# Kernel optimization log

Hardware: AMD Instinct MI355X
Metric: run time of the kernel (lower is better)

Reference implementation:

```python
import jax, jax.numpy as jnp
import numpy as np

B, T, D, H = 4, 2048, 1024, 16
DH = D // H


def setup_inputs() -> dict:
    key = jax.random.key(0)
    ks = jax.random.split(key, 11)
    s = 1.0 / np.sqrt(D)
    return {
        "q": jax.random.normal(ks[0], (B, T, D), jnp.float32),
        "k": jax.random.normal(ks[1], (B, T, D), jnp.float32),
        "v": jax.random.normal(ks[2], (B, T, D), jnp.float32),
        "Wq": jax.random.normal(ks[3], (D, D), jnp.float32) * s,
        "bq": jax.random.normal(ks[4], (D,), jnp.float32) * s,
        "Wk": jax.random.normal(ks[5], (D, D), jnp.float32) * s,
        "bk": jax.random.normal(ks[6], (D,), jnp.float32) * s,
        "Wv": jax.random.normal(ks[7], (D, D), jnp.float32) * s,
        "bv": jax.random.normal(ks[8], (D,), jnp.float32) * s,
        "Wo": jax.random.normal(ks[9], (D, D), jnp.float32) * s,
        "bo": jax.random.normal(ks[10], (D,), jnp.float32) * s,
    }


def _heads(x):
    # (B, T, D) -> (B, H, T, DH)
    return x.reshape(B, T, H, DH).transpose(0, 2, 1, 3)


def reference(q, k, v, Wq, bq, Wk, bk, Wv, bv, Wo, bo):
    qh = _heads(q @ Wq + bq)
    kh = _heads(k @ Wk + bk)
    vh = _heads(v @ Wv + bv)
    scale = 1.0 / np.sqrt(DH).astype(np.float32)
    # full (B, H, T, T) score matrix, as in the original module
    scores = jnp.einsum("bhqd,bhkd->bhqk", qh, kh) * scale
    causal = jnp.tril(jnp.ones((T, T), dtype=bool))  # keep j <= i (causal intent)
    scores = jnp.where(causal, scores, -jnp.inf)
    attn = jax.nn.softmax(scores, axis=-1)
    ctx = jnp.einsum("bhqk,bhkd->bhqd", attn, vh)
    ctx = ctx.transpose(0, 2, 1, 3).reshape(B, T, D)
    return ctx @ Wo + bo
```

## Files before the change

### kernel.cpp

```cpp
#include <hip/hip_runtime.h>
#include <hip/hip_bf16.h>

#define NB 4
#define NT 2048
#define ND 1024
#define NH 16
#define NDH 64
#define NM (NB*NT)

typedef __bf16 bf16_t;
typedef bf16_t bf16x4 __attribute__((ext_vector_type(4)));
typedef bf16_t bf16x8 __attribute__((ext_vector_type(8)));
typedef float f32x2 __attribute__((ext_vector_type(2)));
typedef float f32x4 __attribute__((ext_vector_type(4)));
typedef unsigned int u32x4 __attribute__((ext_vector_type(4)));

__device__ __forceinline__ void gload_lds16(const bf16_t* g, bf16_t* l) {
  __builtin_amdgcn_global_load_lds(
      (const __attribute__((address_space(1))) unsigned int*)g,
      (__attribute__((address_space(3))) unsigned int*)l, 16, 0, 0);
}

__device__ __forceinline__ f32x2 lo2(f32x4 v) { return __builtin_shufflevector(v, v, 0, 1); }
__device__ __forceinline__ f32x2 hi2(f32x4 v) { return __builtin_shufflevector(v, v, 2, 3); }

__device__ __forceinline__ float exp2_hw(float x) {
  float r;
  asm("v_exp_f32 %0, %1" : "=v"(r) : "v"(x));
  return r;
}

__global__ void transpose_cvt4(const float* __restrict__ w0, const float* __restrict__ w1,
                               const float* __restrict__ w2, const float* __restrict__ w3,
                               bf16_t* __restrict__ o0, bf16_t* __restrict__ o1,
                               bf16_t* __restrict__ o2, bf16_t* __restrict__ o3) {
  __shared__ float tile[32][33];
  const float* in = blockIdx.z == 0 ? w0 : blockIdx.z == 1 ? w1 : blockIdx.z == 2 ? w2 : w3;
  bf16_t* out     = blockIdx.z == 0 ? o0 : blockIdx.z == 1 ? o1 : blockIdx.z == 2 ? o2 : o3;
  int n0 = blockIdx.x * 32, k0 = blockIdx.y * 32;
  int tx = threadIdx.x & 31, ty = threadIdx.x >> 5;
  #pragma unroll
  for (int r = ty; r < 32; r += 8)
    tile[r][tx] = in[(size_t)(k0 + r) * ND + n0 + tx];
  __syncthreads();
  #pragma unroll
  for (int r = ty; r < 32; r += 8)
    out[(size_t)(n0 + r) * ND + k0 + tx] = (bf16_t)tile[tx][r];
}

__global__ void cvt3(const float* __restrict__ q, const float* __restrict__ k,
                     const float* __restrict__ v, bf16_t* __restrict__ oq,
                     bf16_t* __restrict__ ok, bf16_t* __restrict__ ov) {
  const float* in = blockIdx.y == 0 ? q : blockIdx.y == 1 ? k : v;
  bf16_t* out     = blockIdx.y == 0 ? oq : blockIdx.y == 1 ? ok : ov;
  int i = blockIdx.x * 256 + threadIdx.x;
  float4 vv = ((const float4*)in)[i];
  bf16x4 o;
  o[0] = (bf16_t)vv.x; o[1] = (bf16_t)vv.y; o[2] = (bf16_t)vv.z; o[3] = (bf16_t)vv.w;
  ((bf16x4*)out)[i] = o;
}


#define GEMM8_CORE(Aptr, Btptr)                                                     \
  const int K = ND;                                                                 \
  const int tid = threadIdx.x, lane = tid & 63, wid = tid >> 6;                     \
  const int wm = wid >> 2, wn = wid & 3;                                            \
  const int lrow = lane & 15, lg = lane >> 4, rb = lg << 2;                         \
  const int tm = blockIdx.y * 128, tn = blockIdx.x * 256;                           \
  const int d0 = tid * 16, d1 = 8192 + tid * 16;                                    \
  const int r0s = d0 >> 7, r1s = d1 >> 7;                                           \
  const int cb0 = (d0 & 127) ^ ((r0s & 7) << 4);                                    \
  const int cb1 = (d1 & 127) ^ ((r1s & 7) << 4);                                    \
  const int e0 = d0 >> 1, e1 = d1 >> 1;                                             \
  const bf16_t* aC0 = (Aptr) + (size_t)(tm + r0s) * K + (cb0 >> 1);                 \
  const bf16_t* aC1 = (Aptr) + (size_t)(tm + r1s) * K + (cb1 >> 1);                 \
  const bf16_t* b0C0 = (Btptr) + (size_t)(tn + r0s) * K + (cb0 >> 1);               \
  const bf16_t* b0C1 = (Btptr) + (size_t)(tn + r1s) * K + (cb1 >> 1);               \
  const bf16_t* b1C0 = b0C0 + (size_t)128 * K;                                      \
  const bf16_t* b1C1 = b0C1 + (size_t)128 * K;                                      \
  const int swzk = (lrow & 7) << 4;                                                 \
  const int kc0 = (lg * 16) ^ swzk;                                                 \
  const int kc1 = (64 + lg * 16) ^ swzk;                                            \
  const int aBase = wm * 8192 + lrow * 128;                                         \
  const int bBase = (wn & 1) * 8192 + lrow * 128;                                   \
  f32x4 acc[4][4];                                                                  \
  _Pragma("unroll")                                                                 \
  for (int m = 0; m < 4; ++m)                                                       \
    _Pragma("unroll")                                                               \
    for (int n = 0; n < 4; ++n) {                                                   \
      f32x4 zz = {0.f, 0.f, 0.f, 0.f};                                              \
      acc[m][n] = zz;                                                               \
    }                                                                               \
                           \
  gload_lds16(aC0,  &S[0][0][0] + e0); gload_lds16(aC1,  &S[0][0][0] + e1);         \
  gload_lds16(b0C0, &S[0][1][0] + e0); gload_lds16(b0C1, &S[0][1][0] + e1);         \
  gload_lds16(b1C0, &S[0][2][0] + e0); gload_lds16(b1C1, &S[0][2][0] + e1);         \
  gload_lds16(b0C0 + 64, &S[1][1][0] + e0); gload_lds16(b0C1 + 64, &S[1][1][0] + e1);\
  gload_lds16(b1C0 + 64, &S[1][2][0] + e0); gload_lds16(b1C1 + 64, &S[1][2][0] + e1);\
  asm volatile("s_waitcnt vmcnt(4)\n\ts_barrier" ::: "memory");                     \
  const int NS = K / 64;                                                            \
  _Pragma("unroll 1")                                                               \
  for (int s = 0; s < NS; ++s) {                                                    \
    const int b = s & 1;                                                            \
    const char* aReg = (const char*)&S[b][0][0];                                    \
    const char* bReg = (const char*)&S[b][1 + (wn >> 1)][0];                        \
                \
    bf16x8 bfr[4][2];                                                               \
    _Pragma("unroll")                                                               \
    for (int n = 0; n < 4; ++n) {                                                   \
      bfr[n][0] = *(const bf16x8*)(bReg + n * 2048 + bBase + kc0);                  \
      bfr[n][1] = *(const bf16x8*)(bReg + n * 2048 + bBase + kc1);                  \
    }                                                                               \
    bf16x8 afrA[2][2];                                                              \
    afrA[0][0] = *(const bf16x8*)(aReg + 0 * 2048 + aBase + kc0);                   \
    afrA[0][1] = *(const bf16x8*)(aReg + 0 * 2048 + aBase + kc1);                   \
    afrA[1][0] = *(const bf16x8*)(aReg + 1 * 2048 + aBase + kc0);                   \
    afrA[1][1] = *(const bf16x8*)(aReg + 1 * 2048 + aBase + kc1);                   \
    if (s + 1 < NS) {                                                               \
      gload_lds16(aC0 + (s + 1) * 64, &S[b ^ 1][0][0] + e0);                        \
      gload_lds16(aC1 + (s + 1) * 64, &S[b ^ 1][0][0] + e1);                        \
    }                                                                               \
    asm volatile("s_barrier" ::: "memory");                                         \
    __builtin_amdgcn_s_setprio(1);                                                  \
    _Pragma("unroll")                                                               \
    for (int mm = 0; mm < 2; ++mm)                                                  \
      _Pragma("unroll")                                                             \
      for (int n = 0; n < 4; ++n)                                                   \
        _Pragma("unroll")                                                           \
        for (int kk = 0; kk < 2; ++kk)                                              \
          acc[mm][n] = __builtin_amdgcn_mfma_f32_16x16x32_bf16(                     \
              afrA[mm][kk], bfr[n][kk], acc[mm][n], 0, 0, 0);                       \
    __builtin_amdgcn_s_setprio(0);                                                  \
    asm volatile("s_waitcnt lgkmcnt(0)\n\ts_barrier" ::: "memory");                 \
                            \
    bf16x8 afrB[2][2];                                                              \
    afrB[0][0] = *(const bf16x8*)(aReg + 2 * 2048 + aBase + kc0);                   \
    afrB[0][1] = *(const bf16x8*)(aReg + 2 * 2048 + aBase + kc1);                   \
    afrB[1][0] = *(const bf16x8*)(aReg + 3 * 2048 + aBase + kc0);                   \
    afrB[1][1] = *(const bf16x8*)(aReg + 3 * 2048 + aBase + kc1);                   \
    if (s + 2 < NS) {                                                               \
      gload_lds16(b0C0 + (s + 2) * 64, &S[b][1][0] + e0);                           \
      gload_lds16(b0C1 + (s + 2) * 64, &S[b][1][0] + e1);                           \
      gload_lds16(b1C0 + (s + 2) * 64, &S[b][2][0] + e0);                           \
      gload_lds16(b1C1 + (s + 2) * 64, &S[b][2][0] + e1);                           \
    }                                                                               \
    asm volatile("s_barrier" ::: "memory");                                         \
    __builtin_amdgcn_s_setprio(1);                                                  \
    _Pragma("unroll")                                                               \
    for (int mm = 0; mm < 2; ++mm)                                                  \
      _Pragma("unroll")                                                             \
      for (int n = 0; n < 4; ++n)                                                   \
        _Pragma("unroll")                                                           \
        for (int kk = 0; kk < 2; ++kk)                                              \
          acc[2 + mm][n] = __builtin_amdgcn_mfma_f32_16x16x32_bf16(                 \
              afrB[mm][kk], bfr[n][kk], acc[2 + mm][n], 0, 0, 0);                   \
    __builtin_amdgcn_s_setprio(0);                                                  \
    if (s < NS - 2)                                                                 \
      asm volatile("s_waitcnt vmcnt(4) lgkmcnt(0)\n\ts_barrier" ::: "memory");      \
    else if (s == NS - 2)                                                           \
      asm volatile("s_waitcnt vmcnt(0) lgkmcnt(0)\n\ts_barrier" ::: "memory");      \
    else                                                                            \
      asm volatile("s_waitcnt lgkmcnt(0)" ::: "memory");                            \
  }

__global__ __launch_bounds__(512, 2) void gemm8_qkv(
    const bf16_t* __restrict__ Aq, const bf16_t* __restrict__ Ak, const bf16_t* __restrict__ Av,
    const bf16_t* __restrict__ Bq, const bf16_t* __restrict__ Bk, const bf16_t* __restrict__ Bv,
    const float* __restrict__ bq, const float* __restrict__ bk, const float* __restrict__ bv,
    bf16_t* __restrict__ Qh, bf16_t* __restrict__ Kh, bf16_t* __restrict__ Vt,
    float qscale) {
  __shared__ bf16_t S[2][3][8192];
  const int z = blockIdx.z;
  const bf16_t* A    = z == 0 ? Aq : z == 1 ? Ak : Av;
  const bf16_t* Bt   = z == 0 ? Bq : z == 1 ? Bk : Bv;
  const float*  bias = z == 0 ? bq : z == 1 ? bk : bv;
  const float   scale = z == 0 ? qscale : 1.0f;
  bf16_t* outp = z == 0 ? Qh : z == 1 ? Kh : Vt;

  GEMM8_CORE(A, Bt)

  #pragma unroll
  for (int n = 0; n < 4; ++n) {
    const int ncol = tn + wn * 64 + n * 16 + lrow;
    const float bv = bias[ncol];
    const int h = ncol >> 6, dh = ncol & (NDH - 1);
    #pragma unroll
    for (int m = 0; m < 4; ++m) {
      const int m0 = tm + wm * 64 + m * 16 + rb;
      const int bb = m0 >> 11, t0 = m0 & (NT - 1);
      if (z == 2) {
        bf16x4 o;
        #pragma unroll
        for (int r = 0; r < 4; ++r) o[r] = (bf16_t)(acc[m][n][r] + bv);
        size_t idx = ((size_t)(bb * NH + h) * NDH + dh) * NT + t0;
        *(bf16x4*)(outp + idx) = o;
      } else {
        #pragma unroll
        for (int r = 0; r < 4; ++r) {
          float val = (acc[m][n][r] + bv) * scale;
          size_t idx = ((size_t)(bb * NH + h) * NT + t0 + r) * NDH + dh;
          outp[idx] = (bf16_t)val;
        }
      }
    }
  }
}

__global__ __launch_bounds__(512, 2) void gemm8_out(
    const bf16_t* __restrict__ A, const bf16_t* __restrict__ Bt,
    const float* __restrict__ bias, float* __restrict__ outp) {
  __shared__ bf16_t S[2][3][8192];

  GEMM8_CORE(A, Bt)

  #pragma unroll
  for (int n = 0; n < 4; ++n) {
    const int ncol = tn + wn * 64 + n * 16 + lrow;
    const float bv = bias[ncol];
    #pragma unroll
    for (int m = 0; m < 4; ++m) {
      const int m0 = tm + wm * 64 + m * 16 + rb;
      #pragma unroll
      for (int r = 0; r < 4; ++r)
        outp[(size_t)(m0 + r) * ND + ncol] = acc[m][n][r] + bv;
    }
  }
}

__device__ __forceinline__ bf16x8 lds_swz_read(const bf16_t* base, int row, int colb) {
  return *(const bf16x8*)((const char*)base + row * 128 + (colb ^ ((row & 7) << 4)));
}

#define CVTPK(lo, hi) ({ unsigned r_; \
  asm("v_cvt_pk_bf16_f32 %0, %1, %2" : "=v"(r_) : "v"(lo), "v"(hi)); r_; })

__global__ __launch_bounds__(256) void attn_kernel(
    const bf16_t* __restrict__ Qh, const bf16_t* __restrict__ Kh,
    const bf16_t* __restrict__ Vt, bf16_t* __restrict__ ctx) {
  __shared__ bf16_t Ks[2][64 * 64];
  __shared__ bf16_t Vs[2][64 * 64];
  const int tid  = threadIdx.x;
  const int lane = tid & 63;
  const int wid  = tid >> 6;

  const int work    = (blockIdx.x & 7) * 128 + (blockIdx.x >> 3);
  const int bh      = work >> 4;
  const int pairIdx = work & 15;
  const int b = bh >> 4, h = bh & 15;

  const bf16_t* Qbh = Qh + (size_t)bh * NT * NDH;
  const bf16_t* Kbh = Kh + (size_t)bh * NT * NDH;
  const bf16_t* Vbh = Vt + (size_t)bh * NDH * NT;

  const int lrow = lane & 15;
  const int lg   = lane >> 4;

  const char *kS0, *kS1, *vS0, *vS1;
  {
    int o0 = wid * 1024 + lane * 16;
    int o1 = 4096 + wid * 1024 + lane * 16;
    int r0_ = o0 >> 7, r1_ = o1 >> 7;
    kS0 = (const char*)Kbh + (o0 ^ ((r0_ & 7) << 4));
    kS1 = (const char*)Kbh + (o1 ^ ((r1_ & 7) << 4));
    int c0 = (o0 & 127) ^ ((r0_ & 7) << 4);
    int c1 = (o1 & 127) ^ ((r1_ & 7) << 4);
    vS0 = (const char*)Vbh + (size_t)r0_ * (NT * 2) + c0;
    vS1 = (const char*)Vbh + (size_t)r1_ * (NT * 2) + c1;
  }
  const int ldsOff = wid * 512;

  auto stage = [&](int t, int buf) {
    bf16_t* kb = Ks[buf];
    bf16_t* vb = Vs[buf];
    size_t kOff = (size_t)t * 8192;
    size_t vOff = (size_t)t * 128;
    gload_lds16((const bf16_t*)(kS0 + kOff), kb + ldsOff);
    gload_lds16((const bf16_t*)(kS1 + kOff), kb + 2048 + ldsOff);
    gload_lds16((const bf16_t*)(vS0 + vOff), vb + ldsOff);
    gload_lds16((const bf16_t*)(vS1 + vOff), vb + 2048 + ldsOff);
  };

  #pragma unroll 1
  for (int half = 0; half < 2; ++half) {
    const int qidx = half ? (31 - pairIdx) : pairIdx;
    const int r0   = qidx * 64 + wid * 16;
    const int qg   = r0 + lrow;

    bf16x8 qf0 = *(const bf16x8*)&Qbh[(size_t)(r0 + lrow) * NDH + lg * 8];
    bf16x8 qf1 = *(const bf16x8*)&Qbh[(size_t)(r0 + lrow) * NDH + 32 + lg * 8];

    float lsum = 0.f;
    f32x4 acc[4];
    #pragma unroll
    for (int d = 0; d < 4; ++d) { f32x4 z = {0.f, 0.f, 0.f, 0.f}; acc[d] = z; }

    __syncthreads();
    stage(0, 0);
    int cur = 0;

    #pragma unroll 1
    for (int t = 0; t <= qidx; ++t) {
      asm volatile("s_waitcnt vmcnt(0)\n\ts_barrier" ::: "memory");
      if (t < qidx) stage(t + 1, cur ^ 1);

      const bf16_t* ksCur = Ks[cur];
      const bf16_t* vsCur = Vs[cur];

      f32x4 sg[4];
      #pragma unroll
      for (int g = 0; g < 4; ++g) { f32x4 z = {0.f, 0.f, 0.f, 0.f}; sg[g] = z; }
      __builtin_amdgcn_s_setprio(1);
      #pragma unroll
      for (int g = 0; g < 4; ++g) {
        bf16x8 kfa = lds_swz_read(ksCur, g * 16 + lrow, lg * 16);
        sg[g] = __builtin_amdgcn_mfma_f32_16x16x32_bf16(kfa, qf0, sg[g], 0, 0, 0);
        bf16x8 kfb = lds_swz_read(ksCur, g * 16 + lrow, 64 + lg * 16);
        sg[g] = __builtin_amdgcn_mfma_f32_16x16x32_bf16(kfb, qf1, sg[g], 0, 0, 0);
      }
      __builtin_amdgcn_s_setprio(0);

      if (t == qidx) {
        const int jb = t * 64;
        #pragma unroll
        for (int g = 0; g < 4; ++g)
          #pragma unroll
          for (int r = 0; r < 4; ++r)
            if (jb + g * 16 + lg * 4 + r > qg) sg[g][r] = -1e30f;
      }

      #pragma unroll
      for (int g = 0; g < 4; ++g)
        #pragma unroll
        for (int r = 0; r < 4; ++r) sg[g][r] = exp2_hw(sg[g][r]);
      f32x2 s2 = (lo2(sg[0]) + hi2(sg[0])) + (lo2(sg[1]) + hi2(sg[1]));
      s2 += (lo2(sg[2]) + hi2(sg[2])) + (lo2(sg[3]) + hi2(sg[3]));
      lsum += s2[0] + s2[1];

      unsigned W00 = CVTPK(sg[0][0], sg[0][1]), W01 = CVTPK(sg[0][2], sg[0][3]);
      unsigned W10 = CVTPK(sg[1][0], sg[1][1]), W11 = CVTPK(sg[1][2], sg[1][3]);
      unsigned W20 = CVTPK(sg[2][0], sg[2][1]), W21 = CVTPK(sg[2][2], sg[2][3]);
      unsigned W30 = CVTPK(sg[3][0], sg[3][1]), W31 = CVTPK(sg[3][2], sg[3][3]);
      unsigned w00, w01, w02, w03, w10, w11, w12, w13;
      { unsigned a = W00, bb = W10;
        asm("v_permlane32_swap_b32 %0, %1" : "+v"(a), "+v"(bb));
        asm("v_permlane16_swap_b32 %0, %1" : "+v"(a), "+v"(bb));
        w00 = a; w02 = bb; }
      { unsigned a = W01, bb = W11;
        asm("v_permlane32_swap_b32 %0, %1" : "+v"(a), "+v"(bb));
        asm("v_permlane16_swap_b32 %0, %1" : "+v"(a), "+v"(bb));
        w01 = a; w03 = bb; }
      { unsigned a = W20, bb = W30;
        asm("v_permlane32_swap_b32 %0, %1" : "+v"(a), "+v"(bb));
        asm("v_permlane16_swap_b32 %0, %1" : "+v"(a), "+v"(bb));
        w10 = a; w12 = bb; }
      { unsigned a = W21, bb = W31;
        asm("v_permlane32_swap_b32 %0, %1" : "+v"(a), "+v"(bb));
        asm("v_permlane16_swap_b32 %0, %1" : "+v"(a), "+v"(bb));
        w11 = a; w13 = bb; }
      u32x4 c0 = {w00, w01, w02, w03};
      u32x4 c1 = {w10, w11, w12, w13};
      bf16x8 pf0 = __builtin_bit_cast(bf16x8, c0);
      bf16x8 pf1 = __builtin_bit_cast(bf16x8, c1);

      __builtin_amdgcn_s_setprio(1);
      #pragma unroll
      for (int d = 0; d < 4; ++d) {
        bf16x8 vf0 = lds_swz_read(vsCur, d * 16 + lrow, lg * 16);
        acc[d] = __builtin_amdgcn_mfma_f32_16x16x32_bf16(vf0, pf0, acc[d], 0, 0, 0);
        bf16x8 vf1 = lds_swz_read(vsCur, d * 16 + lrow, 64 + lg * 16);
        acc[d] = __builtin_amdgcn_mfma_f32_16x16x32_bf16(vf1, pf1, acc[d], 0, 0, 0);
      }
      __builtin_amdgcn_s_setprio(0);

      cur ^= 1;
    }

    float ps = lsum;
    ps += __shfl_xor(ps, 16);
    ps += __shfl_xor(ps, 32);
    float inv = 1.f / ps;
    f32x4 inv4 = {inv, inv, inv, inv};
    size_t orow = ((size_t)b * NT + qg) * ND + h * NDH;
    #pragma unroll
    for (int d2 = 0; d2 < 4; ++d2) {
      f32x4 vv = acc[d2] * inv4;
      bf16x4 o;
      #pragma unroll
      for (int r = 0; r < 4; ++r) o[r] = (bf16_t)vv[r];
      *(bf16x4*)&ctx[orow + d2 * 16 + lg * 4] = o;
    }
  }
}

extern "C" void kernel_launch(void* const* d_in, const int* in_sizes, int n_in,
                              void* d_out, int out_size, void* d_ws, size_t ws_size,
                              hipStream_t stream) {
  const float* q  = (const float*)d_in[0];
  const float* k  = (const float*)d_in[1];
  const float* v  = (const float*)d_in[2];
  const float* Wq = (const float*)d_in[3];
  const float* bq = (const float*)d_in[4];
  const float* Wk = (const float*)d_in[5];
  const float* bk = (const float*)d_in[6];
  const float* Wv = (const float*)d_in[7];
  const float* bv = (const float*)d_in[8];
  const float* Wo = (const float*)d_in[9];
  const float* bo = (const float*)d_in[10];
  float* out = (float*)d_out;

  char* ws = (char*)d_ws;
  const size_t szMK = (size_t)NM * ND * sizeof(bf16_t);
  const size_t szW  = (size_t)ND * ND * sizeof(bf16_t);
  bf16_t* Xq  = (bf16_t*)d_out;
  bf16_t* Xk  = Xq + (size_t)NM * ND;
  bf16_t* Xv  = (bf16_t*)(ws);
  bf16_t* ctx = (bf16_t*)(ws);
  bf16_t* Qh  = (bf16_t*)(ws + szMK);
  bf16_t* Kh  = (bf16_t*)(ws + 2 * szMK);
  bf16_t* Vt  = (bf16_t*)(ws + 3 * szMK);
  bf16_t* Wqt = (bf16_t*)(ws + 4 * szMK);
  bf16_t* Wkt = (bf16_t*)(ws + 4 * szMK + szW);
  bf16_t* Wvt = (bf16_t*)(ws + 4 * szMK + 2 * szW);
  bf16_t* Wot = (bf16_t*)(ws + 4 * szMK + 3 * szW);

  dim3 tb(256);
  transpose_cvt4<<<dim3(ND / 32, ND / 32, 4), tb, 0, stream>>>(Wq, Wk, Wv, Wo,
                                                               Wqt, Wkt, Wvt, Wot);

  const float qscale = 0.125f * 1.44269504f;

  cvt3<<<dim3(NM * ND / 4 / 256, 3), tb, 0, stream>>>(q, k, v, Xq, Xk, Xv);

  gemm8_qkv<<<dim3(ND / 256, NM / 128, 3), dim3(512), 0, stream>>>(
      Xq, Xk, Xv, Wqt, Wkt, Wvt, bq, bk, bv, Qh, Kh, Vt, qscale);

  attn_kernel<<<dim3(NB * NH * 16), tb, 0, stream>>>(Qh, Kh, Vt, ctx);

  gemm8_out<<<dim3(ND / 256, NM / 128), dim3(512), 0, stream>>>(ctx, Wot, bo, out);
}
```

Before: 183.3 us.

## Fuse fp32-to-bf16 input conversion into QKV projection GEMM A-tile loads

The separate cvt3 kernel, which wrote bf16 copies of q/k/v, is removed. The QKV GEMM now loads fp32 A tiles into registers, converts them with packed bf16 conversions, and stores them swizzled into LDS, with a two-stage register prefetch. This removes one full write and read of the bf16 activations plus a kernel launch. In exchange the GEMM reads twice as many A bytes from global memory, and register pressure in the inner loop goes up.

```diff
diff --git a/kernel.cpp b/kernel.cpp
--- a/kernel.cpp
+++ b/kernel.cpp
@@ -29,6 +29,9 @@
   asm("v_exp_f32 %0, %1" : "=v"(r) : "v"(x));
   return r;
 }
+
+#define CVTPK(lo, hi) ({ unsigned r_; \
+  asm("v_cvt_pk_bf16_f32 %0, %1, %2" : "=v"(r_) : "v"(lo), "v"(hi)); r_; })
 
 __global__ void transpose_cvt4(const float* __restrict__ w0, const float* __restrict__ w1,
                                const float* __restrict__ w2, const float* __restrict__ w3,
@@ -48,18 +51,171 @@
     out[(size_t)(n0 + r) * ND + k0 + tx] = (bf16_t)tile[tx][r];
 }
 
-__global__ void cvt3(const float* __restrict__ q, const float* __restrict__ k,
-                     const float* __restrict__ v, bf16_t* __restrict__ oq,
-                     bf16_t* __restrict__ ok, bf16_t* __restrict__ ov) {
-  const float* in = blockIdx.y == 0 ? q : blockIdx.y == 1 ? k : v;
-  bf16_t* out     = blockIdx.y == 0 ? oq : blockIdx.y == 1 ? ok : ov;
-  int i = blockIdx.x * 256 + threadIdx.x;
-  float4 vv = ((const float4*)in)[i];
-  bf16x4 o;
-  o[0] = (bf16_t)vv.x; o[1] = (bf16_t)vv.y; o[2] = (bf16_t)vv.z; o[3] = (bf16_t)vv.w;
-  ((bf16x4*)out)[i] = o;
-}
-
+__global__ __launch_bounds__(512, 2) void gemm8_qkv(
+    const float* __restrict__ Aq, const float* __restrict__ Ak, const float* __restrict__ Av,
+    const bf16_t* __restrict__ Bq, const bf16_t* __restrict__ Bk, const bf16_t* __restrict__ Bv,
+    const float* __restrict__ bq, const float* __restrict__ bk, const float* __restrict__ bv,
+    bf16_t* __restrict__ Qh, bf16_t* __restrict__ Kh, bf16_t* __restrict__ Vt,
+    float qscale) {
+  __shared__ bf16_t S[2][3][8192];
+  const int z = blockIdx.z;
+  const float*  A    = z == 0 ? Aq : z == 1 ? Ak : Av;
+  const bf16_t* Bt   = z == 0 ? Bq : z == 1 ? Bk : Bv;
+  const float*  bias = z == 0 ? bq : z == 1 ? bk : bv;
+  const float   scale = z == 0 ? qscale : 1.0f;
+  bf16_t* outp = z == 0 ? Qh : z == 1 ? Kh : Vt;
+
+  const int K = ND;
+  const int tid = threadIdx.x, lane = tid & 63, wid = tid >> 6;
+  const int wm = wid >> 2, wn = wid & 3;
+  const int lrow = lane & 15, lg = lane >> 4, rb = lg << 2;
+  const int tm = blockIdx.y * 128, tn = blockIdx.x * 256;
+
+  const int d0 = tid * 16, d1 = 8192 + tid * 16;
+  const int r0s = d0 >> 7, r1s = d1 >> 7;
+  const int cb0 = (d0 & 127) ^ ((r0s & 7) << 4);
+  const int cb1 = (d1 & 127) ^ ((r1s & 7) << 4);
+  const int e0 = d0 >> 1, e1 = d1 >> 1;
+  const bf16_t* b0C0 = Bt + (size_t)(tn + r0s) * K + (cb0 >> 1);
+  const bf16_t* b0C1 = Bt + (size_t)(tn + r1s) * K + (cb1 >> 1);
+  const bf16_t* b1C0 = b0C0 + (size_t)128 * K;
+  const bf16_t* b1C1 = b0C1 + (size_t)128 * K;
+
+  const int arow = tid >> 2;
+  const int acolf = (tid & 3) << 4;
+  const float* aF = A + (size_t)(tm + arow) * K + acolf;
+  const int aswz = (arow & 7) << 4;
+  const int wb0 = arow * 128 + ((((tid & 3) << 5))      ^ aswz);
+  const int wb1 = arow * 128 + ((((tid & 3) << 5) + 16) ^ aswz);
+
+  const int swzk = (lrow & 7) << 4;
+  const int kc0 = (lg * 16) ^ swzk;
+  const int kc1 = (64 + lg * 16) ^ swzk;
+  const int aBase = wm * 8192 + lrow * 128;
+  const int bBase = (wn & 1) * 8192 + lrow * 128;
+
+  f32x4 acc[4][4];
+  #pragma unroll
+  for (int m = 0; m < 4; ++m)
+    #pragma unroll
+    for (int n = 0; n < 4; ++n) {
+      f32x4 zz = {0.f, 0.f, 0.f, 0.f};
+      acc[m][n] = zz;
+    }
+
+  float4 ar0, ar1, ar2, ar3;
+  #define LOAD_ARX(off) do { const float4* ap_ = (const float4*)(aF + (off)); \
+    ar0 = ap_[0]; ar1 = ap_[1]; ar2 = ap_[2]; ar3 = ap_[3]; } while (0)
+  #define CVT_WRITE_A(dstBase) do { \
+    u32x4 c0_ = { CVTPK(ar0.x, ar0.y), CVTPK(ar0.z, ar0.w), \
+                  CVTPK(ar1.x, ar1.y), CVTPK(ar1.z, ar1.w) }; \
+    u32x4 c1_ = { CVTPK(ar2.x, ar2.y), CVTPK(ar2.z, ar2.w), \
+                  CVTPK(ar3.x, ar3.y), CVTPK(ar3.z, ar3.w) }; \
+    *(u32x4*)((char*)(dstBase) + wb0) = c0_; \
+    *(u32x4*)((char*)(dstBase) + wb1) = c1_; \
+  } while (0)
+
+  LOAD_ARX(0);
+  gload_lds16(b0C0, &S[0][1][0] + e0); gload_lds16(b0C1, &S[0][1][0] + e1);
+  gload_lds16(b1C0, &S[0][2][0] + e0); gload_lds16(b1C1, &S[0][2][0] + e1);
+  gload_lds16(b0C0 + 64, &S[1][1][0] + e0); gload_lds16(b0C1 + 64, &S[1][1][0] + e1);
+  gload_lds16(b1C0 + 64, &S[1][2][0] + e0); gload_lds16(b1C1 + 64, &S[1][2][0] + e1);
+  CVT_WRITE_A(&S[0][0][0]);
+  LOAD_ARX(64);
+  asm volatile("s_waitcnt vmcnt(8) lgkmcnt(0)\n\ts_barrier" ::: "memory");
+
+  const int NS = K / 64;
+  #pragma unroll 1
+  for (int s = 0; s < NS; ++s) {
+    const int b = s & 1;
+    const char* aReg = (const char*)&S[b][0][0];
+    const char* bReg = (const char*)&S[b][1 + (wn >> 1)][0];
+
+    if (s + 1 < NS) CVT_WRITE_A(&S[(s + 1) & 1][0][0]);
+    if (s + 2 < NS) LOAD_ARX((s + 2) * 64);
+    bf16x8 bfr[4][2];
+    #pragma unroll
+    for (int n = 0; n < 4; ++n) {
+      bfr[n][0] = *(const bf16x8*)(bReg + n * 2048 + bBase + kc0);
+      bfr[n][1] = *(const bf16x8*)(bReg + n * 2048 + bBase + kc1);
+    }
+    bf16x8 afrA[2][2];
+    afrA[0][0] = *(const bf16x8*)(aReg + 0 * 2048 + aBase + kc0);
+    afrA[0][1] = *(const bf16x8*)(aReg + 0 * 2048 + aBase + kc1);
+    afrA[1][0] = *(const bf16x8*)(aReg + 1 * 2048 + aBase + kc0);
+    afrA[1][1] = *(const bf16x8*)(aReg + 1 * 2048 + aBase + kc1);
+    asm volatile("s_barrier" ::: "memory");
+    __builtin_amdgcn_s_setprio(1);
+    #pragma unroll
+    for (int mm = 0; mm < 2; ++mm)
+      #pragma unroll
+      for (int n = 0; n < 4; ++n)
+        #pragma unroll
+        for (int kk = 0; kk < 2; ++kk)
+          acc[mm][n] = __builtin_amdgcn_mfma_f32_16x16x32_bf16(
+              afrA[mm][kk], bfr[n][kk], acc[mm][n], 0, 0, 0);
+    __builtin_amdgcn_s_setprio(0);
+    asm volatile("s_waitcnt lgkmcnt(0)\n\ts_barrier" ::: "memory");
+
+    bf16x8 afrB[2][2];
+    afrB[0][0] = *(const bf16x8*)(aReg + 2 * 2048 + aBase + kc0);
+    afrB[0][1] = *(const bf16x8*)(aReg + 2 * 2048 + aBase + kc1);
+    afrB[1][0] = *(const bf16x8*)(aReg + 3 * 2048 + aBase + kc0);
+    afrB[1][1] = *(const bf16x8*)(aReg + 3 * 2048 + aBase + kc1);
+    if (s + 2 < NS) {
+      gload_lds16(b0C0 + (s + 2) * 64, &S[b][1][0] + e0);
+      gload_lds16(b0C1 + (s + 2) * 64, &S[b][1][0] + e1);
+      gload_lds16(b1C0 + (s + 2) * 64, &S[b][2][0] + e0);
+      gload_lds16(b1C1 + (s + 2) * 64, &S[b][2][0] + e1);
+    }
+    asm volatile("s_barrier" ::: "memory");
+    __builtin_amdgcn_s_setprio(1);
+    #pragma unroll
+    for (int mm = 0; mm < 2; ++mm)
+      #pragma unroll
+      for (int n = 0; n < 4; ++n)
+        #pragma unroll
+        for (int kk = 0; kk < 2; ++kk)
+          acc[2 + mm][n] = __builtin_amdgcn_mfma_f32_16x16x32_bf16(
+              afrB[mm][kk], bfr[n][kk], acc[2 + mm][n], 0, 0, 0);
+    __builtin_amdgcn_s_setprio(0);
+
+    if (s < NS - 2)
+      asm volatile("s_waitcnt vmcnt(8) lgkmcnt(0)\n\ts_barrier" ::: "memory");
+    else if (s == NS - 2)
+      asm volatile("s_waitcnt vmcnt(0) lgkmcnt(0)\n\ts_barrier" ::: "memory");
+    else
+      asm volatile("s_waitcnt lgkmcnt(0)" ::: "memory");
+  }
+  #undef LOAD_ARX
+  #undef CVT_WRITE_A
+
+  #pragma unroll
+  for (int n = 0; n < 4; ++n) {
+    const int ncol = tn + wn * 64 + n * 16 + lrow;
+    const float bv = bias[ncol];
+    const int h = ncol >> 6, dh = ncol & (NDH - 1);
+    #pragma unroll
+    for (int m = 0; m < 4; ++m) {
+      const int m0 = tm + wm * 64 + m * 16 + rb;
+      const int bb = m0 >> 11, t0 = m0 & (NT - 1);
+      if (z == 2) {
+        bf16x4 o;
+        #pragma unroll
+        for (int r = 0; r < 4; ++r) o[r] = (bf16_t)(acc[m][n][r] + bv);
+        size_t idx = ((size_t)(bb * NH + h) * NDH + dh) * NT + t0;
+        *(bf16x4*)(outp + idx) = o;
+      } else {
+        #pragma unroll
+        for (int r = 0; r < 4; ++r) {
+          float val = (acc[m][n][r] + bv) * scale;
+          size_t idx = ((size_t)(bb * NH + h) * NT + t0 + r) * NDH + dh;
+          outp[idx] = (bf16_t)val;
+        }
+      }
+    }
+  }
+}
 
 #define GEMM8_CORE(Aptr, Btptr)                                                     \
   const int K = ND;                                                                 \
@@ -91,7 +247,6 @@
       f32x4 zz = {0.f, 0.f, 0.f, 0.f};                                              \
       acc[m][n] = zz;                                                               \
     }                                                                               \
-                           \
   gload_lds16(aC0,  &S[0][0][0] + e0); gload_lds16(aC1,  &S[0][0][0] + e1);         \
   gload_lds16(b0C0, &S[0][1][0] + e0); gload_lds16(b0C1, &S[0][1][0] + e1);         \
   gload_lds16(b1C0, &S[0][2][0] + e0); gload_lds16(b1C1, &S[0][2][0] + e1);         \
@@ -104,7 +259,6 @@
     const int b = s & 1;                                                            \
     const char* aReg = (const char*)&S[b][0][0];                                    \
     const char* bReg = (const char*)&S[b][1 + (wn >> 1)][0];                        \
-                \
     bf16x8 bfr[4][2];                                                               \
     _Pragma("unroll")                                                               \
     for (int n = 0; n < 4; ++n) {                                                   \
@@ -132,7 +286,6 @@
               afrA[mm][kk], bfr[n][kk], acc[mm][n], 0, 0, 0);                       \
     __builtin_amdgcn_s_setprio(0);                                                  \
     asm volatile("s_waitcnt lgkmcnt(0)\n\ts_barrier" ::: "memory");                 \
-                            \
     bf16x8 afrB[2][2];                                                              \
     afrB[0][0] = *(const bf16x8*)(aReg + 2 * 2048 + aBase + kc0);                   \
     afrB[0][1] = *(const bf16x8*)(aReg + 2 * 2048 + aBase + kc1);                   \
@@ -163,19 +316,10 @@
       asm volatile("s_waitcnt lgkmcnt(0)" ::: "memory");                            \
   }
 
-__global__ __launch_bounds__(512, 2) void gemm8_qkv(
-    const bf16_t* __restrict__ Aq, const bf16_t* __restrict__ Ak, const bf16_t* __restrict__ Av,
-    const bf16_t* __restrict__ Bq, const bf16_t* __restrict__ Bk, const bf16_t* __restrict__ Bv,
-    const float* __restrict__ bq, const float* __restrict__ bk, const float* __restrict__ bv,
-    bf16_t* __restrict__ Qh, bf16_t* __restrict__ Kh, bf16_t* __restrict__ Vt,
-    float qscale) {
+__global__ __launch_bounds__(512, 2) void gemm8_out(
+    const bf16_t* __restrict__ A, const bf16_t* __restrict__ Bt,
+    const float* __restrict__ bias, float* __restrict__ outp) {
   __shared__ bf16_t S[2][3][8192];
-  const int z = blockIdx.z;
-  const bf16_t* A    = z == 0 ? Aq : z == 1 ? Ak : Av;
-  const bf16_t* Bt   = z == 0 ? Bq : z == 1 ? Bk : Bv;
-  const float*  bias = z == 0 ? bq : z == 1 ? bk : bv;
-  const float   scale = z == 0 ? qscale : 1.0f;
-  bf16_t* outp = z == 0 ? Qh : z == 1 ? Kh : Vt;
 
   GEMM8_CORE(A, Bt)
 
@@ -183,43 +327,9 @@
   for (int n = 0; n < 4; ++n) {
     const int ncol = tn + wn * 64 + n * 16 + lrow;
     const float bv = bias[ncol];
-    const int h = ncol >> 6, dh = ncol & (NDH - 1);
     #pragma unroll
     for (int m = 0; m < 4; ++m) {
       const int m0 = tm + wm * 64 + m * 16 + rb;
-      const int bb = m0 >> 11, t0 = m0 & (NT - 1);
-      if (z == 2) {
-        bf16x4 o;
-        #pragma unroll
-        for (int r = 0; r < 4; ++r) o[r] = (bf16_t)(acc[m][n][r] + bv);
-        size_t idx = ((size_t)(bb * NH + h) * NDH + dh) * NT + t0;
-        *(bf16x4*)(outp + idx) = o;
-      } else {
-        #pragma unroll
-        for (int r = 0; r < 4; ++r) {
-          float val = (acc[m][n][r] + bv) * scale;
-          size_t idx = ((size_t)(bb * NH + h) * NT + t0 + r) * NDH + dh;
-          outp[idx] = (bf16_t)val;
-        }
-      }
-    }
-  }
-}
-
-__global__ __launch_bounds__(512, 2) void gemm8_out(
-    const bf16_t* __restrict__ A, const bf16_t* __restrict__ Bt,
-    const float* __restrict__ bias, float* __restrict__ outp) {
-  __shared__ bf16_t S[2][3][8192];
-
-  GEMM8_CORE(A, Bt)
-
-  #pragma unroll
-  for (int n = 0; n < 4; ++n) {
-    const int ncol = tn + wn * 64 + n * 16 + lrow;
-    const float bv = bias[ncol];
-    #pragma unroll
-    for (int m = 0; m < 4; ++m) {
-      const int m0 = tm + wm * 64 + m * 16 + rb;
       #pragma unroll
       for (int r = 0; r < 4; ++r)
         outp[(size_t)(m0 + r) * ND + ncol] = acc[m][n][r] + bv;
@@ -230,9 +340,6 @@
 __device__ __forceinline__ bf16x8 lds_swz_read(const bf16_t* base, int row, int colb) {
   return *(const bf16x8*)((const char*)base + row * 128 + (colb ^ ((row & 7) << 4)));
 }
-
-#define CVTPK(lo, hi) ({ unsigned r_; \
-  asm("v_cvt_pk_bf16_f32 %0, %1, %2" : "=v"(r_) : "v"(lo), "v"(hi)); r_; })
 
 __global__ __launch_bounds__(256) void attn_kernel(
     const bf16_t* __restrict__ Qh, const bf16_t* __restrict__ Kh,
@@ -411,9 +518,6 @@
   char* ws = (char*)d_ws;
   const size_t szMK = (size_t)NM * ND * sizeof(bf16_t);
   const size_t szW  = (size_t)ND * ND * sizeof(bf16_t);
-  bf16_t* Xq  = (bf16_t*)d_out;
-  bf16_t* Xk  = Xq + (size_t)NM * ND;
-  bf16_t* Xv  = (bf16_t*)(ws);
   bf16_t* ctx = (bf16_t*)(ws);
   bf16_t* Qh  = (bf16_t*)(ws + szMK);
   bf16_t* Kh  = (bf16_t*)(ws + 2 * szMK);
@@ -429,10 +533,8 @@
 
   const float qscale = 0.125f * 1.44269504f;
 
-  cvt3<<<dim3(NM * ND / 4 / 256, 3), tb, 0, stream>>>(q, k, v, Xq, Xk, Xv);
-
   gemm8_qkv<<<dim3(ND / 256, NM / 128, 3), dim3(512), 0, stream>>>(
-      Xq, Xk, Xv, Wqt, Wkt, Wvt, bq, bk, bv, Qh, Kh, Vt, qscale);
+      q, k, v, Wqt, Wkt, Wvt, bq, bk, bv, Qh, Kh, Vt, qscale);
 
   attn_kernel<<<dim3(NB * NH * 16), tb, 0, stream>>>(Qh, Kh, Vt, ctx);
 
```

After: 192.9 us. +5.2%, slower.
